# Performance work log

Measured on AMD Instinct MI355X. Metric: run time of the kernel, lower is better.

## Reference

```python
import math
import jax, jax.numpy as jnp
import numpy as np

N_HEADS = 8

def setup_inputs() -> dict:
    key = jax.random.key(0)
    bs, n_heads, ch, l = 4, N_HEADS, 64, 1024
    width = 3 * n_heads * ch      # 1536 (packed q,k,v channels)
    T = 3 * l                     # 3072 (three spatial bands: ll, lh, hl)
    qkv = jax.random.normal(key, (bs, width, T), dtype=jnp.float32)
    return {"qkv": qkv, "l": l}

def reference(qkv, l):
    n_heads = N_HEADS
    bs, width, T = qkv.shape
    ch = width // (3 * n_heads)
    q, k, v = jnp.split(qkv, 3, axis=1)              # each (bs, n_heads*ch, T)
    scale = 1.0 / math.sqrt(math.sqrt(ch))
    qh = (q * scale).reshape(bs * n_heads, ch, T)
    kh = (k * scale).reshape(bs * n_heads, ch, T)
    vh = v.reshape(bs * n_heads, ch, T)
    # The original computes attention separately for q[:, :, :l], [l:2l], [2l:],
    # but k/v (and the softmax axis s) are identical, so computing attention
    # over the full query once and splitting the output is the same math.
    attn = jnp.einsum('bct,bcs->bts', qh, kh)        # (bs*H, T, T)
    w = jax.nn.softmax(attn.astype(jnp.float32), axis=-1).astype(attn.dtype)
    agg = jnp.einsum('bts,bcs->bct', w, vh).reshape(bs, n_heads * ch, T)
    return (agg[:, :, :l], agg[:, :, l:2 * l], agg[:, :, 2 * l:])
```

## Files before the change

### kernel.cpp

```cpp
#include <hip/hip_runtime.h>
#include <hip/hip_bf16.h>
#include <stdint.h>

#define T      3072
#define CH     64
#define HEADS  32
#define BM     128
#define BN     64
#define NIT    (T / BN)

typedef unsigned short u16;
typedef short short8 __attribute__((ext_vector_type(8)));
typedef float floatx4 __attribute__((ext_vector_type(4)));

__device__ __forceinline__ unsigned pk2(float a, float b) {
  union { __hip_bfloat162 h; unsigned u; } cv;
  cv.h = __float22bfloat162_rn(float2{a, b});
  return cv.u;
}

__device__ __forceinline__ void gl_lds16(const void* g, void* l) {
  __builtin_amdgcn_global_load_lds(
      (const __attribute__((address_space(1))) uint32_t*)g,
      (__attribute__((address_space(3))) uint32_t*)l, 16, 0, 0);
}

__device__ __forceinline__ void pl32swap(unsigned& x, unsigned& y) {
#if __has_builtin(__builtin_amdgcn_permlane32_swap)
  auto r = __builtin_amdgcn_permlane32_swap(x, y, false, false);
  x = r[0]; y = r[1];
#else
  asm("v_permlane32_swap_b32 %0, %1" : "+v"(x), "+v"(y));
#endif
}
__device__ __forceinline__ void pl16swap(unsigned& x, unsigned& y) {
#if __has_builtin(__builtin_amdgcn_permlane16_swap)
  auto r = __builtin_amdgcn_permlane16_swap(x, y, false, false);
  x = r[0]; y = r[1];
#else
  asm("v_permlane16_swap_b32 %0, %1" : "+v"(x), "+v"(y));
#endif
}

__global__ __launch_bounds__(256) void qktrans(
    const float* __restrict__ qkv, u16* __restrict__ Qt, u16* __restrict__ Kt,
    u16* __restrict__ Vo) {
  __shared__ __align__(16) u16 tl[64][72];
  const int ttile = blockIdx.x, hh = blockIdx.y, role = blockIdx.z;
  const int b = hh >> 3, h = hh & 7;
  const int t0 = ttile * 64;
  const int tid = threadIdx.x;

  if (role == 2) {
    const float* vsrc = qkv + (size_t)(b * 1536 + 1024 + h * CH) * T;
    u16* vdst = Vo + (size_t)(b * 512 + h * CH) * T;
#pragma unroll
    for (int p = 0; p < 2; ++p) {
      const int r = p * 32 + (tid >> 3);
      const int off = (tid & 7) * 8;
      const float4* s4 = (const float4*)(vsrc + (size_t)r * T + t0 + off);
      float4 a = s4[0], c = s4[1];
      uint4 o;
      o.x = pk2(a.x, a.y); o.y = pk2(a.z, a.w);
      o.z = pk2(c.x, c.y); o.w = pk2(c.z, c.w);
      *(uint4*)(vdst + (size_t)r * T + t0 + off) = o;
    }
    return;
  }

  const float* src = qkv + (size_t)(b * 1536 + role * 512 + h * CH) * T;
  const float scale = (role == 0) ? 0.18033688011112042f : 1.0f;

#pragma unroll
  for (int p = 0; p < 2; ++p) {
    const int c0 = p * 32 + ((tid >> 4) << 1);
    const int ts = (tid & 15) * 4;
    float4 a = *(const float4*)(src + (size_t)c0 * T + t0 + ts);
    float4 c = *(const float4*)(src + (size_t)(c0 + 1) * T + t0 + ts);
    *(unsigned*)&tl[ts + 0][c0] = pk2(a.x * scale, c.x * scale);
    *(unsigned*)&tl[ts + 1][c0] = pk2(a.y * scale, c.y * scale);
    *(unsigned*)&tl[ts + 2][c0] = pk2(a.z * scale, c.z * scale);
    *(unsigned*)&tl[ts + 3][c0] = pk2(a.w * scale, c.w * scale);
  }
  __syncthreads();
  u16* dst = (role == 0 ? Qt : Kt) + (size_t)hh * T * CH;
#pragma unroll
  for (int q = 0; q < 2; ++q) {
    const int t = q * 32 + (tid >> 3);
    const int cc = (tid & 7) * 8;
    uint4 v = *(const uint4*)&tl[t][cc];
    *(uint4*)(dst + (size_t)(t0 + t) * CH + cc) = v;
  }
}

__global__ __launch_bounds__(256, 3) void attn(
    const u16* __restrict__ Qt, const u16* __restrict__ Kt,
    const u16* __restrict__ Vg, float* __restrict__ out) {
  __shared__ __align__(16) u16 KB[3][BN * CH];
  __shared__ __align__(16) u16 VB[3][CH * BN];

  const int qtile = blockIdx.x, hh = blockIdx.y;
  const int tid = threadIdx.x;
  const int wave = tid >> 6, lane = tid & 63;
  const int l15 = lane & 15, quad = lane >> 4;
  const int t0 = qtile * BM + wave * 32;
  const int b = hh >> 3, h = hh & 7;

  const u16* Qh = Qt + (size_t)hh * T * CH;
  const u16* Kh = Kt + (size_t)hh * T * CH;
  const u16* Vh = Vg + (size_t)hh * CH * T;

  short8 qf[2][2];
#pragma unroll
  for (int tq = 0; tq < 2; ++tq)
#pragma unroll
    for (int kc = 0; kc < 2; ++kc)
      qf[tq][kc] = *(const short8*)(Qh + (size_t)(t0 + tq * 16 + l15) * CH + kc * 32 + quad * 8);

  const short8 ones = {0x3F80, 0x3F80, 0x3F80, 0x3F80, 0x3F80, 0x3F80, 0x3F80, 0x3F80};

  floatx4 oacc[2][4] = {};
  floatx4 lacc[2] = {};

  int sr[2], sc[2];
#pragma unroll
  for (int j = 0; j < 2; ++j) {
    const int p = j * 256 + wave * 64 + lane;
    sr[j] = p >> 3;
    sc[j] = (p & 7) ^ ((sr[j] + 2 * (sr[j] >> 3)) & 7);
  }
  const int swl = (l15 + 2 * (l15 >> 3)) & 7;

#define STAGE(buf, s0)                                                              \
  do {                                                                              \
    _Pragma("unroll")                                                               \
    for (int j = 0; j < 2; ++j)                                                     \
      gl_lds16(Kh + (size_t)((s0) + sr[j]) * CH + sc[j] * 8,                        \
               &KB[buf][(j * 256 + wave * 64) * 8]);                                \
    _Pragma("unroll")                                                               \
    for (int j = 0; j < 2; ++j)                                                     \
      gl_lds16(Vh + (size_t)sr[j] * T + (s0) + sc[j] * 8,                           \
               &VB[buf][(j * 256 + wave * 64) * 8]);                                \
  } while (0)

  STAGE(0, 0);
  STAGE(1, BN);

  int cur = 0, nxt = 2;
  for (int it = 0; it < NIT; ++it) {
    if (it + 1 < NIT) {
      asm volatile("s_waitcnt vmcnt(4)" ::: "memory");
    } else {
      asm volatile("s_waitcnt vmcnt(0)" ::: "memory");
    }
    __builtin_amdgcn_s_barrier();
    __builtin_amdgcn_sched_barrier(0);
    if (it + 2 < NIT) STAGE(nxt, (it + 2) * BN);

    const u16* KL = KB[cur];
    const u16* VL = VB[cur];

    floatx4 sacc[2][4];
    __builtin_amdgcn_s_setprio(1);
#pragma unroll
    for (int nt = 0; nt < 4; ++nt) {
      const int ph0 = quad ^ swl ^ ((nt & 1) * 4);
      const int base = (nt * 16 + l15) * CH;
      const short8 kf0 = *(const short8*)(KL + base + ph0 * 8);
      const short8 kf1 = *(const short8*)(KL + base + (ph0 ^ 4) * 8);
#pragma unroll
      for (int tq = 0; tq < 2; ++tq) {
        floatx4 z = {0.f, 0.f, 0.f, 0.f};
        z = __builtin_amdgcn_mfma_f32_16x16x32_bf16(kf0, qf[tq][0], z, 0, 0, 0);
        z = __builtin_amdgcn_mfma_f32_16x16x32_bf16(kf1, qf[tq][1], z, 0, 0, 0);
        sacc[tq][nt] = z;
      }
    }
    __builtin_amdgcn_s_setprio(0);

    unsigned Apk[2][4], Bpk[2][4];
#pragma unroll
    for (int tq = 0; tq < 2; ++tq)
#pragma unroll
      for (int nt = 0; nt < 4; ++nt) {
        floatx4 sv = sacc[tq][nt];
        float p0 = __builtin_amdgcn_exp2f(sv[0]);
        float p1 = __builtin_amdgcn_exp2f(sv[1]);
        float p2 = __builtin_amdgcn_exp2f(sv[2]);
        float p3 = __builtin_amdgcn_exp2f(sv[3]);
        Apk[tq][nt] = pk2(p0, p1);
        Bpk[tq][nt] = pk2(p2, p3);
      }

    __builtin_amdgcn_s_setprio(1);
#pragma unroll
    for (int ks = 0; ks < 2; ++ks) {
      short8 pf[2];
#pragma unroll
      for (int tq = 0; tq < 2; ++tq) {
        unsigned a0 = Apk[tq][2 * ks], a1 = Apk[tq][2 * ks + 1];
        unsigned b0 = Bpk[tq][2 * ks], b1 = Bpk[tq][2 * ks + 1];
        pl32swap(a0, a1); pl16swap(a0, a1);
        pl32swap(b0, b1); pl16swap(b0, b1);
        union { uint4 u; short8 s; } pw;
        pw.u.x = a0; pw.u.y = b0; pw.u.z = a1; pw.u.w = b1;
        pf[tq] = pw.s;
        lacc[tq] = __builtin_amdgcn_mfma_f32_16x16x32_bf16(pf[tq], ones, lacc[tq], 0, 0, 0);
      }
#pragma unroll
      for (int mt = 0; mt < 4; ++mt) {
        const int ph = quad ^ swl ^ ((mt & 1) * 4) ^ (ks * 4);
        const short8 vf = *(const short8*)(VL + (mt * 16 + l15) * BN + ph * 8);
        oacc[0][mt] = __builtin_amdgcn_mfma_f32_16x16x32_bf16(pf[0], vf, oacc[0][mt], 0, 0, 0);
        oacc[1][mt] = __builtin_amdgcn_mfma_f32_16x16x32_bf16(pf[1], vf, oacc[1][mt], 0, 0, 0);
      }
    }
    __builtin_amdgcn_s_setprio(0);

    cur = (cur == 2) ? 0 : cur + 1;
    nxt = (nxt == 2) ? 0 : nxt + 1;
  }

  float linv[2][4];
#pragma unroll
  for (int tq = 0; tq < 2; ++tq)
#pragma unroll
    for (int r = 0; r < 4; ++r) linv[tq][r] = 1.0f / lacc[tq][r];

#pragma unroll
  for (int tq = 0; tq < 2; ++tq) {
    const int tgr = t0 + tq * 16 + quad * 4;
    const int band = tgr >> 10, tt = tgr & 1023;
    float* obase = out + (size_t)band * (4 * 512 * 1024)
                       + (size_t)b * (512 * 1024)
                       + (size_t)(h * CH) * 1024 + tt;
#pragma unroll
    for (int mt = 0; mt < 4; ++mt) {
      const int c = mt * 16 + l15;
      float4 v;
      v.x = oacc[tq][mt][0] * linv[tq][0];
      v.y = oacc[tq][mt][1] * linv[tq][1];
      v.z = oacc[tq][mt][2] * linv[tq][2];
      v.w = oacc[tq][mt][3] * linv[tq][3];
      *(float4*)(obase + (size_t)c * 1024) = v;
    }
  }
}

extern "C" void kernel_launch(void* const* d_in, const int* in_sizes, int n_in,
                              void* d_out, int out_size, void* d_ws, size_t ws_size,
                              hipStream_t stream) {
  (void)in_sizes; (void)n_in; (void)out_size; (void)ws_size;
  const float* qkv = (const float*)d_in[0];
  u16* Qt = (u16*)d_ws;
  u16* Kt = Qt + (size_t)HEADS * T * CH;
  u16* Vo = Kt + (size_t)HEADS * T * CH;
  float* out = (float*)d_out;

  qktrans<<<dim3(T / 64, HEADS, 3), 256, 0, stream>>>(qkv, Qt, Kt, Vo);
  attn<<<dim3(T / BM, HEADS), 256, 0, stream>>>(Qt, Kt, Vo, out);
}
```

Measured before the change: 210.9 us.

## Split key dimension across two wave groups with LDS reduction of partial outputs

Doubles the attention block to 512 threads. Each group of four waves handles half of every 64-key tile, and each thread issues half as many async LDS loads. At the end, the second group writes its partial output and row-sum accumulators to shared memory, and the first group adds them and writes the normalized result. The aim is more waves per query tile for latency hiding, at the cost of extra barriers, an LDS reduction, and idle waves during the epilogue.

```diff
diff --git a/kernel.cpp b/kernel.cpp
--- a/kernel.cpp
+++ b/kernel.cpp
@@ -93,17 +93,19 @@
   }
 }
 
-__global__ __launch_bounds__(256, 3) void attn(
+__global__ __launch_bounds__(512, 6) void attn(
     const u16* __restrict__ Qt, const u16* __restrict__ Kt,
     const u16* __restrict__ Vg, float* __restrict__ out) {
-  __shared__ __align__(16) u16 KB[3][BN * CH];
-  __shared__ __align__(16) u16 VB[3][CH * BN];
+  __shared__ __align__(16) u16 SMEM[24576];
+  u16* KBp = SMEM;
+  u16* VBp = SMEM + 12288;
 
   const int qtile = blockIdx.x, hh = blockIdx.y;
   const int tid = threadIdx.x;
   const int wave = tid >> 6, lane = tid & 63;
+  const int tg = wave & 3, sg = wave >> 2;
   const int l15 = lane & 15, quad = lane >> 4;
-  const int t0 = qtile * BM + wave * 32;
+  const int t0 = qtile * BM + tg * 32;
   const int b = hh >> 3, h = hh & 7;
 
   const u16* Qh = Qt + (size_t)hh * T * CH;
@@ -122,25 +124,15 @@
   floatx4 oacc[2][4] = {};
   floatx4 lacc[2] = {};
 
-  int sr[2], sc[2];
-#pragma unroll
-  for (int j = 0; j < 2; ++j) {
-    const int p = j * 256 + wave * 64 + lane;
-    sr[j] = p >> 3;
-    sc[j] = (p & 7) ^ ((sr[j] + 2 * (sr[j] >> 3)) & 7);
-  }
+  const int sr = tid >> 3;
+  const int sc = (tid & 7) ^ ((sr + 2 * (sr >> 3)) & 7);
   const int swl = (l15 + 2 * (l15 >> 3)) & 7;
+  const int wsl = (wave * 64) * 8;
 
 #define STAGE(buf, s0)                                                              \
   do {                                                                              \
-    _Pragma("unroll")                                                               \
-    for (int j = 0; j < 2; ++j)                                                     \
-      gl_lds16(Kh + (size_t)((s0) + sr[j]) * CH + sc[j] * 8,                        \
-               &KB[buf][(j * 256 + wave * 64) * 8]);                                \
-    _Pragma("unroll")                                                               \
-    for (int j = 0; j < 2; ++j)                                                     \
-      gl_lds16(Vh + (size_t)sr[j] * T + (s0) + sc[j] * 8,                           \
-               &VB[buf][(j * 256 + wave * 64) * 8]);                                \
+    gl_lds16(Kh + (size_t)((s0) + sr) * CH + sc * 8, &KBp[(buf) * 4096 + wsl]);     \
+    gl_lds16(Vh + (size_t)sr * T + (s0) + sc * 8, &VBp[(buf) * 4096 + wsl]);        \
   } while (0)
 
   STAGE(0, 0);
@@ -149,7 +141,7 @@
   int cur = 0, nxt = 2;
   for (int it = 0; it < NIT; ++it) {
     if (it + 1 < NIT) {
-      asm volatile("s_waitcnt vmcnt(4)" ::: "memory");
+      asm volatile("s_waitcnt vmcnt(2)" ::: "memory");
     } else {
       asm volatile("s_waitcnt vmcnt(0)" ::: "memory");
     }
@@ -157,15 +149,15 @@
     __builtin_amdgcn_sched_barrier(0);
     if (it + 2 < NIT) STAGE(nxt, (it + 2) * BN);
 
-    const u16* KL = KB[cur];
-    const u16* VL = VB[cur];
-
-    floatx4 sacc[2][4];
+    const u16* KL = KBp + cur * 4096;
+    const u16* VL = VBp + cur * 4096;
+
+    floatx4 sacc[2][2];
     __builtin_amdgcn_s_setprio(1);
 #pragma unroll
-    for (int nt = 0; nt < 4; ++nt) {
-      const int ph0 = quad ^ swl ^ ((nt & 1) * 4);
-      const int base = (nt * 16 + l15) * CH;
+    for (int nt = 0; nt < 2; ++nt) {
+      const int ph0 = quad ^ swl ^ (nt * 4);
+      const int base = (sg * 32 + nt * 16 + l15) * CH;
       const short8 kf0 = *(const short8*)(KL + base + ph0 * 8);
       const short8 kf1 = *(const short8*)(KL + base + (ph0 ^ 4) * 8);
 #pragma unroll
@@ -178,11 +170,11 @@
     }
     __builtin_amdgcn_s_setprio(0);
 
-    unsigned Apk[2][4], Bpk[2][4];
+    unsigned Apk[2][2], Bpk[2][2];
 #pragma unroll
     for (int tq = 0; tq < 2; ++tq)
 #pragma unroll
-      for (int nt = 0; nt < 4; ++nt) {
+      for (int nt = 0; nt < 2; ++nt) {
         floatx4 sv = sacc[tq][nt];
         float p0 = __builtin_amdgcn_exp2f(sv[0]);
         float p1 = __builtin_amdgcn_exp2f(sv[1]);
@@ -193,27 +185,24 @@
       }
 
     __builtin_amdgcn_s_setprio(1);
-#pragma unroll
-    for (int ks = 0; ks < 2; ++ks) {
-      short8 pf[2];
-#pragma unroll
-      for (int tq = 0; tq < 2; ++tq) {
-        unsigned a0 = Apk[tq][2 * ks], a1 = Apk[tq][2 * ks + 1];
-        unsigned b0 = Bpk[tq][2 * ks], b1 = Bpk[tq][2 * ks + 1];
-        pl32swap(a0, a1); pl16swap(a0, a1);
-        pl32swap(b0, b1); pl16swap(b0, b1);
-        union { uint4 u; short8 s; } pw;
-        pw.u.x = a0; pw.u.y = b0; pw.u.z = a1; pw.u.w = b1;
-        pf[tq] = pw.s;
-        lacc[tq] = __builtin_amdgcn_mfma_f32_16x16x32_bf16(pf[tq], ones, lacc[tq], 0, 0, 0);
-      }
-#pragma unroll
-      for (int mt = 0; mt < 4; ++mt) {
-        const int ph = quad ^ swl ^ ((mt & 1) * 4) ^ (ks * 4);
-        const short8 vf = *(const short8*)(VL + (mt * 16 + l15) * BN + ph * 8);
-        oacc[0][mt] = __builtin_amdgcn_mfma_f32_16x16x32_bf16(pf[0], vf, oacc[0][mt], 0, 0, 0);
-        oacc[1][mt] = __builtin_amdgcn_mfma_f32_16x16x32_bf16(pf[1], vf, oacc[1][mt], 0, 0, 0);
-      }
+    short8 pf[2];
+#pragma unroll
+    for (int tq = 0; tq < 2; ++tq) {
+      unsigned a0 = Apk[tq][0], a1 = Apk[tq][1];
+      unsigned b0 = Bpk[tq][0], b1 = Bpk[tq][1];
+      pl32swap(a0, a1); pl16swap(a0, a1);
+      pl32swap(b0, b1); pl16swap(b0, b1);
+      union { uint4 u; short8 s; } pw;
+      pw.u.x = a0; pw.u.y = b0; pw.u.z = a1; pw.u.w = b1;
+      pf[tq] = pw.s;
+      lacc[tq] = __builtin_amdgcn_mfma_f32_16x16x32_bf16(pf[tq], ones, lacc[tq], 0, 0, 0);
+    }
+#pragma unroll
+    for (int mt = 0; mt < 4; ++mt) {
+      const int ph = quad ^ swl ^ ((mt & 1) * 4) ^ (sg * 4);
+      const short8 vf = *(const short8*)(VL + (mt * 16 + l15) * BN + ph * 8);
+      oacc[0][mt] = __builtin_amdgcn_mfma_f32_16x16x32_bf16(pf[0], vf, oacc[0][mt], 0, 0, 0);
+      oacc[1][mt] = __builtin_amdgcn_mfma_f32_16x16x32_bf16(pf[1], vf, oacc[1][mt], 0, 0, 0);
     }
     __builtin_amdgcn_s_setprio(0);
 
@@ -221,28 +210,51 @@
     nxt = (nxt == 2) ? 0 : nxt + 1;
   }
 
-  float linv[2][4];
-#pragma unroll
-  for (int tq = 0; tq < 2; ++tq)
-#pragma unroll
-    for (int r = 0; r < 4; ++r) linv[tq][r] = 1.0f / lacc[tq][r];
-
-#pragma unroll
-  for (int tq = 0; tq < 2; ++tq) {
-    const int tgr = t0 + tq * 16 + quad * 4;
-    const int band = tgr >> 10, tt = tgr & 1023;
-    float* obase = out + (size_t)band * (4 * 512 * 1024)
-                       + (size_t)b * (512 * 1024)
-                       + (size_t)(h * CH) * 1024 + tt;
-#pragma unroll
-    for (int mt = 0; mt < 4; ++mt) {
-      const int c = mt * 16 + l15;
-      float4 v;
-      v.x = oacc[tq][mt][0] * linv[tq][0];
-      v.y = oacc[tq][mt][1] * linv[tq][1];
-      v.z = oacc[tq][mt][2] * linv[tq][2];
-      v.w = oacc[tq][mt][3] * linv[tq][3];
-      *(float4*)(obase + (size_t)c * 1024) = v;
+  __syncthreads();
+  float* CMB = (float*)SMEM;
+  float* reg = CMB + tg * 2560;
+  if (sg == 1) {
+#pragma unroll
+    for (int tq = 0; tq < 2; ++tq) {
+#pragma unroll
+      for (int mt = 0; mt < 4; ++mt)
+        *(floatx4*)(reg + ((tq * 5 + mt) * 64 + lane) * 4) = oacc[tq][mt];
+      *(floatx4*)(reg + ((tq * 5 + 4) * 64 + lane) * 4) = lacc[tq];
+    }
+  }
+  __syncthreads();
+  if (sg == 0) {
+#pragma unroll
+    for (int tq = 0; tq < 2; ++tq) {
+#pragma unroll
+      for (int mt = 0; mt < 4; ++mt)
+        oacc[tq][mt] += *(const floatx4*)(reg + ((tq * 5 + mt) * 64 + lane) * 4);
+      lacc[tq] += *(const floatx4*)(reg + ((tq * 5 + 4) * 64 + lane) * 4);
+    }
+
+    float linv[2][4];
+#pragma unroll
+    for (int tq = 0; tq < 2; ++tq)
+#pragma unroll
+      for (int r = 0; r < 4; ++r) linv[tq][r] = 1.0f / lacc[tq][r];
+
+#pragma unroll
+    for (int tq = 0; tq < 2; ++tq) {
+      const int tgr = t0 + tq * 16 + quad * 4;
+      const int band = tgr >> 10, tt = tgr & 1023;
+      float* obase = out + (size_t)band * (4 * 512 * 1024)
+                         + (size_t)b * (512 * 1024)
+                         + (size_t)(h * CH) * 1024 + tt;
+#pragma unroll
+      for (int mt = 0; mt < 4; ++mt) {
+        const int c = mt * 16 + l15;
+        float4 v;
+        v.x = oacc[tq][mt][0] * linv[tq][0];
+        v.y = oacc[tq][mt][1] * linv[tq][1];
+        v.z = oacc[tq][mt][2] * linv[tq][2];
+        v.w = oacc[tq][mt][3] * linv[tq][3];
+        *(float4*)(obase + (size_t)c * 1024) = v;
+      }
     }
   }
 }
@@ -258,5 +270,5 @@
   float* out = (float*)d_out;
 
   qktrans<<<dim3(T / 64, HEADS, 3), 256, 0, stream>>>(qkv, Qt, Kt, Vo);
-  attn<<<dim3(T / BM, HEADS), 256, 0, stream>>>(Qt, Kt, Vo, out);
-}
+  attn<<<dim3(T / BM, HEADS), 512, 0, stream>>>(Qt, Kt, Vo, out);
+}
```

After: 276.0 us. 30.9% more time.
